# Kernel optimization log

Hardware: AMD Instinct MI355X
Metric: run time of the kernel (lower is better)

Reference implementation:

```python
import jax, jax.numpy as jnp
import numpy as np
from jax import lax

START_IDX = 7
STOP_IDX = 8
TAGSET = 9
VOCAB = 50257
EMB = 512
HID = 1024  # bidirectional: HID//2 per direction
SEQ = 8192


def _lstm_dir(x, Wih, Whh, bih, bhh, reverse):
    # x: [T, EMB]; Wih: [4H, EMB]; Whh: [4H, H]
    H = Whh.shape[1]
    xproj = x @ Wih.T + bih  # big GEMM hoisted out of the scan: [T, 4H]

    def step(carry, xp):
        h, c = carry
        g = xp + h @ Whh.T + bhh
        i, f, gg, o = jnp.split(g, 4)
        i = jax.nn.sigmoid(i)
        f = jax.nn.sigmoid(f)
        gg = jnp.tanh(gg)
        o = jax.nn.sigmoid(o)
        c = f * c + i * gg
        h = o * jnp.tanh(c)
        return (h, c), h

    init = (jnp.zeros((H,), x.dtype), jnp.zeros((H,), x.dtype))
    _, hs = lax.scan(step, init, xproj, reverse=reverse)
    return hs  # [T, H]


def _viterbi(feats, transitions):
    # feats: [T, TAGSET]; transitions[next, prev]
    init = jnp.full((TAGSET,), -10000.0, feats.dtype).at[START_IDX].set(0.0)

    def step(fv, feat):
        scores = fv[None, :] + transitions       # [next, prev]
        bp = jnp.argmax(scores, axis=1)          # best prev per next tag
        fv_new = jnp.max(scores, axis=1) + feat
        return fv_new, bp

    fv, bptrs = lax.scan(step, init, feats)
    terminal = fv + transitions[STOP_IDX]
    best = jnp.argmax(terminal)
    path_score = terminal[best]

    def back(c, bp):
        return bp[c], c

    _, path = lax.scan(back, best, bptrs, reverse=True)  # path[t] = tag at t
    return path_score, path.astype(jnp.int32)


def setup_inputs() -> dict:
    key = jax.random.key(0)
    ks = jax.random.split(key, 13)
    H = HID // 2
    s = lambda *sh: 0.05
    inp = {
        'sentence': jax.random.randint(ks[0], (SEQ,), 0, VOCAB, dtype=jnp.int32),
        'emb': jax.random.normal(ks[1], (VOCAB + 100, EMB), jnp.float32) * 0.05,
        'Wih_f': jax.random.normal(ks[2], (4 * H, EMB), jnp.float32) * 0.05,
        'Whh_f': jax.random.normal(ks[3], (4 * H, H), jnp.float32) * 0.05,
        'bih_f': jnp.zeros((4 * H,), jnp.float32),
        'bhh_f': jnp.zeros((4 * H,), jnp.float32),
        'Wih_b': jax.random.normal(ks[4], (4 * H, EMB), jnp.float32) * 0.05,
        'Whh_b': jax.random.normal(ks[5], (4 * H, H), jnp.float32) * 0.05,
        'bih_b': jnp.zeros((4 * H,), jnp.float32),
        'bhh_b': jnp.zeros((4 * H,), jnp.float32),
        'W_out': jax.random.normal(ks[6], (TAGSET, HID), jnp.float32) * 0.05,
        'b_out': jnp.zeros((TAGSET,), jnp.float32),
    }
    trans = jax.random.normal(ks[7], (TAGSET, TAGSET), jnp.float32)
    trans = trans.at[START_IDX, :].set(-10000.0)
    trans = trans.at[:, STOP_IDX].set(-10000.0)
    inp['transitions'] = trans
    return inp


def reference(sentence, emb, Wih_f, Whh_f, bih_f, bhh_f, Wih_b, Whh_b, bih_b, bhh_b, W_out, b_out, transitions):
    x = emb[sentence]                                   # [T, EMB]
    h_f = _lstm_dir(x, Wih_f, Whh_f, bih_f, bhh_f, reverse=False)
    h_b = _lstm_dir(x, Wih_b, Whh_b, bih_b, bhh_b, reverse=True)
    lstm_out = jnp.concatenate([h_f, h_b], axis=-1)     # [T, HID]
    feats = lstm_out @ W_out.T + b_out                  # [T, TAGSET]
    score, path = _viterbi(feats, transitions)
    return score, path
```

## Files before the change

kernel.cpp:

```cpp
#include <hip/hip_runtime.h>
#include <hip/hip_bf16.h>


#define T_SEQ   8192
#define EMB     512
#define HDIM    512
#define POISON64 0x7F7F7F7F7F7F7F7Full

#define ALOAD_SYS(p)     __hip_atomic_load((p), __ATOMIC_RELAXED, __HIP_MEMORY_SCOPE_SYSTEM)
#define ASTORE_SYS(p, v) __hip_atomic_store((p), (v), __ATOMIC_RELAXED, __HIP_MEMORY_SCOPE_SYSTEM)

__global__ __launch_bounds__(256) void gemm_xproj(
    const int* __restrict__ sentence, const float* __restrict__ emb,
    const float* __restrict__ Wih_f, const float* __restrict__ Wih_b,
    const float* __restrict__ bih_f, const float* __restrict__ bhh_f,
    const float* __restrict__ bih_b, const float* __restrict__ bhh_b,
    float* __restrict__ xprojb)
{
    __shared__ float As[16][132];
    __shared__ float Bs[16][132];
    __shared__ int   srow[128];

    const int tid = threadIdx.x;
    const int bm = blockIdx.x;
    const int bn = blockIdx.y;
    const int fwd = (bn < 16);
    const float* __restrict__ W = fwd ? Wih_f : Wih_b;
    const int jbase = bn * 128 - (fwd ? 0 : 2048);

    if (tid < 128) srow[tid] = sentence[bm * 128 + tid];
    __syncthreads();

    const int lkk = tid & 15;
    const int lr  = tid >> 4;
    int sr[8];
    #pragma unroll
    for (int i = 0; i < 8; ++i) sr[i] = srow[lr * 8 + i];
    const float* wbase = W + (size_t)(jbase + lr * 8) * EMB + lkk;

    const int tx = tid & 15, ty = tid >> 4;
    float acc[8][8] = {};

    for (int kb = 0; kb < 32; ++kb) {
        const int k0 = kb * 16;
        #pragma unroll
        for (int i = 0; i < 8; ++i) {
            As[lkk][lr * 8 + i] = emb[(size_t)sr[i] * EMB + k0 + lkk];
            Bs[lkk][lr * 8 + i] = wbase[(size_t)i * EMB + k0];
        }
        __syncthreads();
        #pragma unroll
        for (int kk = 0; kk < 16; ++kk) {
            const float4 a0 = *(const float4*)&As[kk][ty * 8];
            const float4 a1 = *(const float4*)&As[kk][ty * 8 + 4];
            const float4 b0 = *(const float4*)&Bs[kk][tx * 8];
            const float4 b1 = *(const float4*)&Bs[kk][tx * 8 + 4];
            const float av[8] = {a0.x,a0.y,a0.z,a0.w,a1.x,a1.y,a1.z,a1.w};
            const float bv[8] = {b0.x,b0.y,b0.z,b0.w,b1.x,b1.y,b1.z,b1.w};
            #pragma unroll
            for (int i = 0; i < 8; ++i)
                #pragma unroll
                for (int j = 0; j < 8; ++j)
                    acc[i][j] = fmaf(av[i], bv[j], acc[i][j]);
        }
        __syncthreads();
    }

    const float* b1p = fwd ? bih_f : bih_b;
    const float* b2p = fwd ? bhh_f : bhh_b;
    float bias[8];
    #pragma unroll
    for (int j = 0; j < 8; ++j) {
        const int jj = jbase + tx * 8 + j;
        bias[j] = b1p[jj] + b2p[jj];
    }
    #pragma unroll
    for (int i = 0; i < 8; ++i) {
        const int t = bm * 128 + ty * 8 + i;
        float4* dst = (float4*)&xprojb[(size_t)t * 4096 + bn * 128 + tx * 8];
        dst[0] = make_float4(acc[i][0] + bias[0], acc[i][1] + bias[1],
                             acc[i][2] + bias[2], acc[i][3] + bias[3]);
        dst[1] = make_float4(acc[i][4] + bias[4], acc[i][5] + bias[5],
                             acc[i][6] + bias[6], acc[i][7] + bias[7]);
    }
}

__device__ __forceinline__ float fsig(float x) { return 1.0f / (1.0f + __expf(-x)); }
__device__ __forceinline__ float ftanh(float x) {
    const float e = __expf(-2.0f * fabsf(x));
    return copysignf((1.0f - e) / (1.0f + e), x);
}
__device__ __forceinline__ unsigned long long pack2(float a, float b) {
    return (unsigned long long)__float_as_uint(a) |
           ((unsigned long long)__float_as_uint(b) << 32);
}
__device__ __forceinline__ float2 unpack2(unsigned long long u) {
    return make_float2(__uint_as_float((unsigned)(u & 0xffffffffull)),
                       __uint_as_float((unsigned)(u >> 32)));
}

__global__ __launch_bounds__(256, 1) void lstm_scan(
    const float* __restrict__ xprojb,
    const float* __restrict__ Whh_f, const float* __restrict__ Whh_b,
    float* __restrict__ hseq)
{
    const int tid  = threadIdx.x;
    const int lane = tid & 63;
    const int wv   = tid >> 6;
    const int blk  = blockIdx.x;
    const int dir  = blk & 1;
    const int sub  = blk >> 1;
    const float* __restrict__ Whh = dir ? Whh_b : Whh_f;
    float* hs = hseq + (size_t)dir * T_SEQ * HDIM;

    const int jm = lane >> 4;
    const int ks = lane & 15;
    const int m  = wv * 4 + jm;

    float wr[4][32];
    #pragma unroll
    for (int g = 0; g < 4; ++g) {
        const float* src = Whh + (size_t)(g * 512 + sub * 16 + m) * 512 + ks * 32;
        #pragma unroll
        for (int i = 0; i < 8; ++i) {
            const float4 v = *(const float4*)(src + 4 * i);
            wr[g][4*i] = v.x; wr[g][4*i+1] = v.y; wr[g][4*i+2] = v.z; wr[g][4*i+3] = v.w;
        }
    }

    __shared__ __align__(16) float hsh[2][16][36];

    const bool gl = (ks == 0);
    const float* xrbase = xprojb + (size_t)dir * 2048 + sub * 16 + m;
    float c_state = 0.0f;

    float xp0 = 0.f, xp1 = 0.f, xp2 = 0.f, xp3 = 0.f;
    if (gl) {
        const int t0 = dir ? (T_SEQ - 1) : 0;
        const float* xr = xrbase + (size_t)t0 * 4096;
        xp0 = xr[0]; xp1 = xr[512]; xp2 = xr[1024]; xp3 = xr[1536];
    }

    #pragma unroll 1
    for (int s = 0; s < T_SEQ; ++s) {
        const int t = dir ? (T_SEQ - 1 - s) : s;
        const int p = s & 1;

        float2 hv2;
        if (s == 0) {
            hv2 = make_float2(0.f, 0.f);
        } else {
            const int tprev = dir ? (t + 1) : (t - 1);
            const unsigned long long* hp =
                (const unsigned long long*)(hs + (size_t)tprev * HDIM) + wv * 64 + lane;
            unsigned long long u = ALOAD_SYS(hp);
            while (u == POISON64) u = ALOAD_SYS(hp);
            hv2 = unpack2(u);
        }
        *(float2*)&hsh[p][wv * 4 + (lane >> 4)][2 * (lane & 15)] = hv2;

        asm volatile("s_waitcnt lgkmcnt(0)\n\ts_barrier" ::: "memory");
        __builtin_amdgcn_sched_barrier(0);

        float a0 = 0.f, a1 = 0.f, a2 = 0.f, a3 = 0.f;
        const float4* h4 = (const float4*)&hsh[p][ks][0];
        #pragma unroll
        for (int i = 0; i < 8; ++i) {
            const float4 hv = h4[i];
            a0 = fmaf(wr[0][4*i],   hv.x, a0); a1 = fmaf(wr[1][4*i],   hv.x, a1);
            a2 = fmaf(wr[2][4*i],   hv.x, a2); a3 = fmaf(wr[3][4*i],   hv.x, a3);
            a0 = fmaf(wr[0][4*i+1], hv.y, a0); a1 = fmaf(wr[1][4*i+1], hv.y, a1);
            a2 = fmaf(wr[2][4*i+1], hv.y, a2); a3 = fmaf(wr[3][4*i+1], hv.y, a3);
            a0 = fmaf(wr[0][4*i+2], hv.z, a0); a1 = fmaf(wr[1][4*i+2], hv.z, a1);
            a2 = fmaf(wr[2][4*i+2], hv.z, a2); a3 = fmaf(wr[3][4*i+2], hv.z, a3);
            a0 = fmaf(wr[0][4*i+3], hv.w, a0); a1 = fmaf(wr[1][4*i+3], hv.w, a1);
            a2 = fmaf(wr[2][4*i+3], hv.w, a2); a3 = fmaf(wr[3][4*i+3], hv.w, a3);
        }
        #pragma unroll
        for (int d = 1; d <= 8; d <<= 1) {
            a0 += __shfl_xor(a0, d); a1 += __shfl_xor(a1, d);
            a2 += __shfl_xor(a2, d); a3 += __shfl_xor(a3, d);
        }

        float h = 0.f;
        if (gl) {
            const float i_ = fsig(a0 + xp0);
            const float f_ = fsig(a1 + xp1);
            const float g_ = ftanh(a2 + xp2);
            const float o_ = fsig(a3 + xp3);
            c_state = fmaf(f_, c_state, i_ * g_);
            h = o_ * ftanh(c_state);
        }
        const float ha = __shfl(h, (lane * 32) & 63);
        const float hb = __shfl(h, (lane * 32 + 16) & 63);
        if (lane < 2) {
            unsigned long long* hdst =
                (unsigned long long*)(hs + (size_t)t * HDIM + sub * 16 + wv * 4);
            ASTORE_SYS(hdst + lane, pack2(ha, hb));
        }

        if (gl && s + 1 < T_SEQ) {
            const int tn = dir ? (t - 1) : (t + 1);
            const float* xr = xrbase + (size_t)tn * 4096;
            xp0 = xr[0]; xp1 = xr[512]; xp2 = xr[1024]; xp3 = xr[1536];
        }
    }
}

__global__ __launch_bounds__(256) void feats_kernel(
    const float* __restrict__ hseq, const float* __restrict__ W_out,
    const float* __restrict__ b_out, float* __restrict__ feats)
{
    const int idx = blockIdx.x * 256 + threadIdx.x;
    if (idx >= T_SEQ * 9) return;
    const int t = idx / 9;
    const int n = idx - t * 9;
    const float4* hf = (const float4*)(hseq + (size_t)t * HDIM);
    const float4* hb = (const float4*)(hseq + (size_t)(T_SEQ + t) * HDIM);
    const float4* wf = (const float4*)(W_out + (size_t)n * 1024);
    const float4* wb = wf + 128;
    float acc = b_out[n];
    #pragma unroll 8
    for (int i = 0; i < 128; ++i) {
        const float4 a = hf[i], w = wf[i];
        acc = fmaf(a.x, w.x, acc); acc = fmaf(a.y, w.y, acc);
        acc = fmaf(a.z, w.z, acc); acc = fmaf(a.w, w.w, acc);
    }
    #pragma unroll 8
    for (int i = 0; i < 128; ++i) {
        const float4 a = hb[i], w = wb[i];
        acc = fmaf(a.x, w.x, acc); acc = fmaf(a.y, w.y, acc);
        acc = fmaf(a.z, w.z, acc); acc = fmaf(a.w, w.w, acc);
    }
    feats[idx] = acc;
}

__global__ __launch_bounds__(64) void viterbi_kernel(
    const float* __restrict__ feats, const float* __restrict__ trans,
    unsigned long long* __restrict__ bpw, float* __restrict__ out)
{
    const int lane = threadIdx.x;
    __shared__ __align__(16) float flds[1024 * 9];
    __shared__ unsigned char path_lds[T_SEQ];

    float tr[9];
    #pragma unroll
    for (int p = 0; p < 9; ++p) tr[p] = 0.f;
    float tstop = 0.f;
    if (lane < 9) {
        #pragma unroll
        for (int p = 0; p < 9; ++p) tr[p] = trans[lane * 9 + p];
        tstop = trans[8 * 9 + lane];
    }
    float fv = (lane == 7) ? 0.0f : -10000.0f;

    for (int ch = 0; ch < 8; ++ch) {
        const float4* src = (const float4*)(feats + (size_t)ch * 9216);
        #pragma unroll
        for (int i = 0; i < 36; ++i)
            ((float4*)flds)[lane + i * 64] = src[lane + i * 64];
        __syncthreads();

        for (int tt = 0; tt < 1024; ++tt) {
            const int t = ch * 1024 + tt;
            const float f0 = __shfl(fv, 0), f1 = __shfl(fv, 1), f2 = __shfl(fv, 2);
            const float f3 = __shfl(fv, 3), f4 = __shfl(fv, 4), f5 = __shfl(fv, 5);
            const float f6 = __shfl(fv, 6), f7 = __shfl(fv, 7), f8 = __shfl(fv, 8);
            const float s0 = f0 + tr[0], s1 = f1 + tr[1], s2 = f2 + tr[2];
            const float s3 = f3 + tr[3], s4 = f4 + tr[4], s5 = f5 + tr[5];
            const float s6 = f6 + tr[6], s7 = f7 + tr[7], s8 = f8 + tr[8];
            const float mx = fmaxf(fmaxf(fmaxf(fmaxf(s0, s1), fmaxf(s2, s3)),
                                         fmaxf(fmaxf(s4, s5), fmaxf(s6, s7))), s8);
            const unsigned bits =
                (s0 >= mx ? 1u : 0u)   | (s1 >= mx ? 2u : 0u)   | (s2 >= mx ? 4u : 0u) |
                (s3 >= mx ? 8u : 0u)   | (s4 >= mx ? 16u : 0u)  | (s5 >= mx ? 32u : 0u) |
                (s6 >= mx ? 64u : 0u)  | (s7 >= mx ? 128u : 0u) | (s8 >= mx ? 256u : 0u);
            const int bi = __ffs(bits) - 1;
            const float feat = (lane < 9) ? flds[tt * 9 + lane] : 0.0f;
            fv = mx + feat;
            const unsigned long long b0 = __ballot(bi & 1);
            const unsigned long long b1 = __ballot(bi & 2);
            const unsigned long long b2 = __ballot(bi & 4);
            const unsigned long long b3 = __ballot(bi & 8);
            if (lane == 0) {
                bpw[t] = (b0 & 511ull) | ((b1 & 511ull) << 9) |
                         ((b2 & 511ull) << 18) | ((b3 & 511ull) << 27);
            }
        }
        __syncthreads();
    }

    const float term = fv + tstop;
    const float t0 = __shfl(term, 0), t1 = __shfl(term, 1), t2 = __shfl(term, 2);
    const float t3 = __shfl(term, 3), t4 = __shfl(term, 4), t5 = __shfl(term, 5);
    const float t6 = __shfl(term, 6), t7 = __shfl(term, 7), t8 = __shfl(term, 8);
    const float mxt = fmaxf(fmaxf(fmaxf(fmaxf(t0, t1), fmaxf(t2, t3)),
                                  fmaxf(fmaxf(t4, t5), fmaxf(t6, t7))), t8);
    const unsigned bitst =
        (t0 >= mxt ? 1u : 0u)   | (t1 >= mxt ? 2u : 0u)   | (t2 >= mxt ? 4u : 0u) |
        (t3 >= mxt ? 8u : 0u)   | (t4 >= mxt ? 16u : 0u)  | (t5 >= mxt ? 32u : 0u) |
        (t6 >= mxt ? 64u : 0u)  | (t7 >= mxt ? 128u : 0u) | (t8 >= mxt ? 256u : 0u);
    const int best = __ffs(bitst) - 1;

    if (lane == 0) {
        out[0] = mxt;
        int c = best;
        path_lds[T_SEQ - 1] = (unsigned char)c;
        for (int thi = T_SEQ - 2; thi >= 15; thi -= 16) {
            const int tlo = thi - 15;
            unsigned long long wbuf[16];
            #pragma unroll
            for (int i = 0; i < 16; ++i) wbuf[i] = bpw[tlo + 1 + i];
            #pragma unroll
            for (int i = 15; i >= 0; --i) {
                const unsigned long long wvv = wbuf[i];
                c = (int)((wvv >> c) & 1ull) |
                    ((int)((wvv >> (9 + c)) & 1ull) << 1) |
                    ((int)((wvv >> (18 + c)) & 1ull) << 2) |
                    ((int)((wvv >> (27 + c)) & 1ull) << 3);
                path_lds[tlo + i] = (unsigned char)c;
            }
        }
        for (int t2i = 14; t2i >= 0; --t2i) {
            const unsigned long long wvv = bpw[t2i + 1];
            c = (int)((wvv >> c) & 1ull) |
                ((int)((wvv >> (9 + c)) & 1ull) << 1) |
                ((int)((wvv >> (18 + c)) & 1ull) << 2) |
                ((int)((wvv >> (27 + c)) & 1ull) << 3);
            path_lds[t2i] = (unsigned char)c;
        }
    }
    __syncthreads();
    #pragma unroll 4
    for (int i = 0; i < T_SEQ / 64; ++i) {
        const int t = i * 64 + lane;
        out[1 + t] = (float)path_lds[t];
    }
}

extern "C" void kernel_launch(void* const* d_in, const int* in_sizes, int n_in,
                              void* d_out, int out_size, void* d_ws, size_t ws_size,
                              hipStream_t stream)
{
    (void)in_sizes; (void)n_in; (void)out_size; (void)ws_size;

    const int*   sentence = (const int*)  d_in[0];
    const float* emb      = (const float*)d_in[1];
    const float* Wih_f    = (const float*)d_in[2];
    const float* Whh_f    = (const float*)d_in[3];
    const float* bih_f    = (const float*)d_in[4];
    const float* bhh_f    = (const float*)d_in[5];
    const float* Wih_b    = (const float*)d_in[6];
    const float* Whh_b    = (const float*)d_in[7];
    const float* bih_b    = (const float*)d_in[8];
    const float* bhh_b    = (const float*)d_in[9];
    const float* W_out    = (const float*)d_in[10];
    const float* b_out    = (const float*)d_in[11];
    const float* trans    = (const float*)d_in[12];

    float* ws      = (float*)d_ws;
    float* xprojb  = ws;
    float* hseq    = ws + (size_t)T_SEQ * 4096;
    float* feats   = hseq + (size_t)2 * T_SEQ * HDIM;
    unsigned long long* bpw = (unsigned long long*)(feats + (size_t)T_SEQ * 9);

    hipMemsetAsync(hseq, 0x7F, (size_t)2 * T_SEQ * HDIM * sizeof(float), stream);

    gemm_xproj<<<dim3(64, 32), 256, 0, stream>>>(
        sentence, emb, Wih_f, Wih_b, bih_f, bhh_f, bih_b, bhh_b, xprojb);

    lstm_scan<<<dim3(64), 256, 0, stream>>>(
        xprojb, Whh_f, Whh_b, hseq);

    feats_kernel<<<dim3((T_SEQ * 9 + 255) / 256), 256, 0, stream>>>(
        hseq, W_out, b_out, feats);

    viterbi_kernel<<<dim3(1), 64, 0, stream>>>(feats, trans, bpw, (float*)d_out);
}
```

Baseline: 20.01 ms.

## Pin each LSTM direction to one XCD via ticketed roles and agent-scope atomics

The scan kernel is launched with far more blocks than it needs. Each block reads its hardware XCD id, and blocks on XCD 0 take forward-direction roles while blocks on XCD 1 take backward ones, handed out by atomic tickets. Surplus blocks exit. Keeping each direction's 32 cooperating blocks on one XCD is meant to keep the h-vector exchange in a shared L2, and the atomics are narrowed from system to agent scope to cut coherence cost. The risks are a fallback path that relies on sleeping, possible cross-XCD visibility problems at agent scope if the fallback is used, and the extra launch and ticket overhead.

```diff
diff --git a/kernel.cpp b/kernel.cpp
--- a/kernel.cpp
+++ b/kernel.cpp
@@ -7,8 +7,8 @@
 #define HDIM    512
 #define POISON64 0x7F7F7F7F7F7F7F7Full
 
-#define ALOAD_SYS(p)     __hip_atomic_load((p), __ATOMIC_RELAXED, __HIP_MEMORY_SCOPE_SYSTEM)
-#define ASTORE_SYS(p, v) __hip_atomic_store((p), (v), __ATOMIC_RELAXED, __HIP_MEMORY_SCOPE_SYSTEM)
+#define ALOAD(p)     __hip_atomic_load((p), __ATOMIC_RELAXED, __HIP_MEMORY_SCOPE_AGENT)
+#define ASTORE(p, v) __hip_atomic_store((p), (v), __ATOMIC_RELAXED, __HIP_MEMORY_SCOPE_AGENT)
 
 __global__ __launch_bounds__(256) void gemm_xproj(
     const int* __restrict__ sentence, const float* __restrict__ emb,
@@ -102,14 +102,32 @@
 __global__ __launch_bounds__(256, 1) void lstm_scan(
     const float* __restrict__ xprojb,
     const float* __restrict__ Whh_f, const float* __restrict__ Whh_b,
-    float* __restrict__ hseq)
+    float* __restrict__ hseq, int* __restrict__ tickets)
 {
     const int tid  = threadIdx.x;
     const int lane = tid & 63;
     const int wv   = tid >> 6;
-    const int blk  = blockIdx.x;
-    const int dir  = blk & 1;
-    const int sub  = blk >> 1;
+
+    __shared__ int role;
+    if (tid == 0) {
+        const int xcd = __builtin_amdgcn_s_getreg(6164) & 7;
+        int d = -1, slot = -1;
+        if (xcd == 0)      { d = 0; slot = atomicAdd(&tickets[0], 1); }
+        else if (xcd == 1) { d = 1; slot = atomicAdd(&tickets[1], 1); }
+        if (slot < 0 || slot >= 32) {
+            for (int i = 0; i < 48; ++i) __builtin_amdgcn_s_sleep(127);
+            d = 0; slot = atomicAdd(&tickets[0], 1);
+            if (slot >= 32) { d = 1; slot = atomicAdd(&tickets[1], 1); }
+            if (slot >= 32) d = -1;
+        }
+        role = (d < 0) ? -1 : (d * 32 + slot);
+    }
+    __syncthreads();
+    const int myrole = role;
+    if (myrole < 0) return;
+    const int dir = myrole >> 5;
+    const int sub = myrole & 31;
+
     const float* __restrict__ Whh = dir ? Whh_b : Whh_f;
     float* hs = hseq + (size_t)dir * T_SEQ * HDIM;
 
@@ -153,8 +171,8 @@
             const int tprev = dir ? (t + 1) : (t - 1);
             const unsigned long long* hp =
                 (const unsigned long long*)(hs + (size_t)tprev * HDIM) + wv * 64 + lane;
-            unsigned long long u = ALOAD_SYS(hp);
-            while (u == POISON64) u = ALOAD_SYS(hp);
+            unsigned long long u = ALOAD(hp);
+            while (u == POISON64) u = ALOAD(hp);
             hv2 = unpack2(u);
         }
         *(float2*)&hsh[p][wv * 4 + (lane >> 4)][2 * (lane & 15)] = hv2;
@@ -196,7 +214,7 @@
         if (lane < 2) {
             unsigned long long* hdst =
                 (unsigned long long*)(hs + (size_t)t * HDIM + sub * 16 + wv * 4);
-            ASTORE_SYS(hdst + lane, pack2(ha, hb));
+            ASTORE(hdst + lane, pack2(ha, hb));
         }
 
         if (gl && s + 1 < T_SEQ) {
@@ -363,14 +381,16 @@
     float* hseq    = ws + (size_t)T_SEQ * 4096;
     float* feats   = hseq + (size_t)2 * T_SEQ * HDIM;
     unsigned long long* bpw = (unsigned long long*)(feats + (size_t)T_SEQ * 9);
+    int* tickets   = (int*)(bpw + T_SEQ);
 
     hipMemsetAsync(hseq, 0x7F, (size_t)2 * T_SEQ * HDIM * sizeof(float), stream);
+    hipMemsetAsync(tickets, 0, 16 * sizeof(int), stream);
 
     gemm_xproj<<<dim3(64, 32), 256, 0, stream>>>(
         sentence, emb, Wih_f, Wih_b, bih_f, bhh_f, bih_b, bhh_b, xprojb);
 
-    lstm_scan<<<dim3(64), 256, 0, stream>>>(
-        xprojb, Whh_f, Whh_b, hseq);
+    lstm_scan<<<dim3(512), 256, 0, stream>>>(
+        xprojb, Whh_f, Whh_b, hseq, tickets);
 
     feats_kernel<<<dim3((T_SEQ * 9 + 255) / 256), 256, 0, stream>>>(
         hseq, W_out, b_out, feats);
```

After: 24.96 ms. +24.7%, slower.
